# Kernel optimization log

Hardware: AMD Instinct MI355X
Metric: run time of the kernel (lower is better)

Reference implementation:

```python
import jax, jax.numpy as jnp
import numpy as np

B, LC, LT, D = 32, 2048, 512, 256  # D = 2*hidden_dim (bidirectional LSTM output)


def setup_inputs() -> dict:
    key = jax.random.key(0)
    k1, k2 = jax.random.split(key)
    return {
        "context_hidden": jax.random.normal(k1, (B, LC, D), dtype=jnp.float32),
        "target_hidden": jax.random.normal(k2, (B, LT, D), dtype=jnp.float32),
    }


def reference(context_hidden, target_hidden):
    # Pairwise Euclidean distance via |c|^2 + |t|^2 - 2 c.t (replaces the
    # original Python double for-loop of per-pair torch.norm calls).
    c2 = jnp.sum(context_hidden * context_hidden, axis=-1, keepdims=True)      # [B,Lc,1]
    t2 = jnp.sum(target_hidden * target_hidden, axis=-1)[:, None, :]           # [B,1,Lt]
    ct = jnp.einsum('bcd,btd->bct', context_hidden, target_hidden)             # [B,Lc,Lt]
    dist = jnp.sqrt(jnp.maximum(c2 + t2 - 2.0 * ct, 0.0))
    weights = 1.0 / (1.0 + dist)  # G2CT: [B,Lc,Lt]
    # G2C_m = weights @ target ; G2T_m = weights^T @ context (as in forward)
    g2c_m = jnp.einsum('bct,btd->bcd', weights, target_hidden)                 # [B,Lc,D]
    g2t_m = jnp.einsum('bct,bcd->btd', weights, context_hidden)                # [B,Lt,D]
    # concat along sequence axis so the block has a single output tensor
    return jnp.concatenate([g2c_m, g2t_m], axis=1)                             # [B,Lc+Lt,D]
```

## Files before the change

kernel.cpp:

```cpp
#include <hip/hip_runtime.h>

typedef float f32x4 __attribute__((ext_vector_type(4)));
typedef short s16x8 __attribute__((ext_vector_type(8)));

#define NB_    32
#define NLC    2048
#define NLT    512
#define ND     256
#define NCHUNK 512
#define NITER  (NCHUNK / 32)

__device__ __forceinline__ unsigned short f2bf(float f) {
    union { float f; unsigned int u; } v; v.f = f;
    unsigned int r = v.u + 0x7FFFu + ((v.u >> 16) & 1u);
    return (unsigned short)(r >> 16);
}

__device__ __forceinline__ s16x8 cvt8(float4 a, float4 c, float s) {
    s16x8 f;
    f[0]=(short)f2bf(s*a.x); f[1]=(short)f2bf(s*a.y); f[2]=(short)f2bf(s*a.z); f[3]=(short)f2bf(s*a.w);
    f[4]=(short)f2bf(s*c.x); f[5]=(short)f2bf(s*c.y); f[6]=(short)f2bf(s*c.z); f[7]=(short)f2bf(s*c.w);
    return f;
}

__device__ __forceinline__ void glds16(const void* g, void* l) {
    __builtin_amdgcn_global_load_lds(
        (const __attribute__((address_space(1))) unsigned int*)g,
        (__attribute__((address_space(3))) unsigned int*)l, 16, 0, 0);
}

__global__ __launch_bounds__(256) void prep_kernel(
    const float* __restrict__ ctx, const float* __restrict__ tgt,
    float* __restrict__ norms,
    unsigned short* __restrict__ ctxb, unsigned short* __restrict__ tgtb)
{
    const int wave = threadIdx.x >> 6;
    const int lane = threadIdx.x & 63;
    const int rid = blockIdx.x * 4 + wave;
    const float* row;
    unsigned short* drow;
    if (rid < NB_ * NLC) { row = ctx + (size_t)rid * ND; drow = ctxb + (size_t)rid * ND; }
    else { row = tgt + (size_t)(rid - NB_ * NLC) * ND; drow = tgtb + (size_t)(rid - NB_ * NLC) * ND; }
    const float4 v = *(const float4*)(row + lane * 4);
    *(ushort4*)(drow + lane * 4) = make_ushort4(f2bf(v.x), f2bf(v.y), f2bf(v.z), f2bf(v.w));
    float s = v.x * v.x + v.y * v.y + v.z * v.z + v.w * v.w;
    #pragma unroll
    for (int off = 32; off >= 1; off >>= 1) s += __shfl_xor(s, off);
    if (lane == 0) norms[rid] = s;
}

__global__ __launch_bounds__(256) void transpose_bf(
    const unsigned short* __restrict__ ctxb, const unsigned short* __restrict__ tgtb,
    unsigned short* __restrict__ ctxTp, unsigned short* __restrict__ tgtTp)
{
    __shared__ unsigned short tile[64][72];
    const int id = blockIdx.x;
    const unsigned short* in;
    unsigned short* outp;
    const int t = threadIdx.x;
    if (id < 4096) {
        const int b = id >> 7, r = id & 127, lt = r >> 2, dt = r & 3;
        in   = ctxb + ((size_t)b * NLC + lt * 64) * ND + dt * 64;
        outp = ctxTp + (((size_t)b * 32 + lt) * 256 + dt * 64) * 64;
    } else {
        const int id2 = id - 4096;
        const int b = id2 >> 5, r = id2 & 31, lt = r >> 2, dt = r & 3;
        in   = tgtb + ((size_t)b * NLT + lt * 64) * ND + dt * 64;
        outp = tgtTp + (((size_t)b * 8 + lt) * 256 + dt * 64) * 64;
    }
    const int r0 = t >> 2, c0 = t & 3;
    const s16x8 v0 = *(const s16x8*)&in[(size_t)r0 * ND + c0 * 8];
    const s16x8 v1 = *(const s16x8*)&in[(size_t)r0 * ND + (c0 + 4) * 8];
    *(s16x8*)&tile[r0][c0 * 8] = v0;
    *(s16x8*)&tile[r0][(c0 + 4) * 8] = v1;
    __syncthreads();
    unsigned short buf[16];
    #pragma unroll
    for (int i = 0; i < 16; ++i) buf[i] = tile[(t & 3) * 16 + i][t >> 2];
    unsigned short* op = outp + (size_t)(t >> 2) * 64 + (t & 3) * 16;
    *(s16x8*)&op[0] = *(const s16x8*)&buf[0];
    *(s16x8*)&op[8] = *(const s16x8*)&buf[8];
}

__global__ __launch_bounds__(256, 2) void k1_weights(
    const unsigned short* __restrict__ ctxb, const unsigned short* __restrict__ tgtb,
    const float* __restrict__ norms,
    unsigned short* __restrict__ Wg, unsigned short* __restrict__ WTg)
{
    __shared__ __align__(16) unsigned short Alds[2][128 * 64];
    __shared__ __align__(16) unsigned short Blds[2][128 * 64];
    __shared__ __align__(16) unsigned short relay[4][16 * 128];

    const int phys = blockIdx.x;
    const int L = (phys & 7) * 256 + (phys >> 3);
    const int b = L >> 6;
    const int r = L & 63;
    const int cb = r >> 2, tb = r & 3;

    const int tid = threadIdx.x, wave = tid >> 6, lane = tid & 63;
    const int lr = lane & 15, lq = lane >> 4;
    const int cw = cb * 128 + wave * 32;

    const unsigned short* Actx = ctxb + ((size_t)b * NLC + cb * 128) * ND;
    const unsigned short* Btgt = tgtb + ((size_t)b * NLT + tb * 128) * ND;

    auto STAGE = [&](int buf, int ks) {
        #pragma unroll
        for (int i = 0; i < 4; ++i) {
            const int q = wave * 4 + i;
            const int rloc = q * 8 + (lane >> 3);
            const int gcol = (lane & 7) ^ (rloc & 7);
            glds16(Actx + (size_t)rloc * ND + ks * 64 + gcol * 8, &Alds[buf][q * 512]);
            glds16(Btgt + (size_t)rloc * ND + ks * 64 + gcol * 8, &Blds[buf][q * 512]);
        }
    };

    f32x4 acc[2][8];
    #pragma unroll
    for (int mf = 0; mf < 2; ++mf)
        #pragma unroll
        for (int nf = 0; nf < 8; ++nf) acc[mf][nf] = (f32x4)(0.0f);

    STAGE(0, 0);
    int buf = 0;
    for (int ks = 0; ks < 4; ++ks) {
        __syncthreads();
        if (ks < 3) STAGE(buf ^ 1, ks + 1);
        #pragma unroll
        for (int kk = 0; kk < 2; ++kk) {
            s16x8 af[2];
            #pragma unroll
            for (int mf = 0; mf < 2; ++mf) {
                const int row = wave * 32 + mf * 16 + lr;
                af[mf] = *(const s16x8*)&Alds[buf][row * 64 + (((kk * 4 + lq) ^ (row & 7)) * 8)];
            }
            #pragma unroll
            for (int nf = 0; nf < 8; ++nf) {
                const int row = nf * 16 + lr;
                const s16x8 bf = *(const s16x8*)&Blds[buf][row * 64 + (((kk * 4 + lq) ^ (row & 7)) * 8)];
                acc[0][nf] = __builtin_amdgcn_mfma_f32_16x16x32_bf16(af[0], bf, acc[0][nf], 0, 0, 0);
                acc[1][nf] = __builtin_amdgcn_mfma_f32_16x16x32_bf16(af[1], bf, acc[1][nf], 0, 0, 0);
            }
        }
        buf ^= 1;
    }

    float c2[2][4], t2[8];
    #pragma unroll
    for (int mf = 0; mf < 2; ++mf)
        #pragma unroll
        for (int j = 0; j < 4; ++j)
            c2[mf][j] = norms[b * NLC + cw + mf * 16 + lq * 4 + j];
    #pragma unroll
    for (int nf = 0; nf < 8; ++nf)
        t2[nf] = norms[NB_ * NLC + b * NLT + tb * 128 + nf * 16 + lr];

    __syncthreads();
    unsigned short* WTs = (unsigned short*)Alds;

    #pragma unroll
    for (int mf = 0; mf < 2; ++mf) {
        #pragma unroll
        for (int nf = 0; nf < 8; ++nf) {
            unsigned short w4[4];
            #pragma unroll
            for (int j = 0; j < 4; ++j) {
                float d2 = c2[mf][j] + t2[nf] - 2.0f * acc[mf][nf][j];
                d2 = d2 > 0.0f ? d2 : 0.0f;
                w4[j] = f2bf(__builtin_amdgcn_rcpf(1.0f + __builtin_amdgcn_sqrtf(d2)));
                const int row = lq * 4 + j;
                relay[wave][row * 128 + ((nf * 16 + lr) ^ ((row & 7) << 3))] = w4[j];
            }
            const int t = nf * 16 + lr;
            const int c4 = (wave * 32 + mf * 16 + lq * 4) ^ ((t & 15) << 3);
            *(ushort4*)&WTs[t * 128 + c4] = make_ushort4(w4[0], w4[1], w4[2], w4[3]);
        }
        __syncthreads();
        {
            const int rrow = lane >> 2;
            const int ts   = (lane >> 1) & 1;
            const int half = lane & 1;
            const size_t wbase =
                (((size_t)b * 8 + tb * 2 + ts) * NLC + cb * 128 + wave * 32 + mf * 16 + rrow) * 64
                + half * 32;
            #pragma unroll
            for (int e = 0; e < 4; ++e) {
                const int tcol = ts * 64 + half * 32 + e * 8;
                const s16x8 v = *(const s16x8*)&relay[wave][rrow * 128 + (tcol ^ ((rrow & 7) << 3))];
                *(s16x8*)&Wg[wbase + e * 8] = v;
            }
        }
        __syncthreads();
    }

    {
        const int trow = tid >> 1;
        const int seg  = tid & 1;
        const size_t wtbase =
            (((size_t)b * 32 + cb * 2 + seg) * NLT + tb * 128 + trow) * 64;
        #pragma unroll
        for (int e = 0; e < 8; ++e) {
            const int c8 = (seg * 64 + e * 8) ^ ((trow & 15) << 3);
            *(s16x8*)&WTg[wtbase + e * 8] = *(const s16x8*)&WTs[trow * 128 + c8];
        }
    }
}

__global__ __launch_bounds__(256, 2) void k2_gemm(
    const unsigned short* __restrict__ Atp, const unsigned short* __restrict__ Wp,
    float* __restrict__ outp)
{
    __shared__ __align__(16) unsigned short Slds[2][256 * 64];

    const int phys = blockIdx.x;
    const int L = (phys & 7) * 64 + (phys >> 3);
    const int b = L >> 4, cb = L & 15;
    float* outB = outp + ((size_t)b * (NLC + NLT) + cb * 128) * ND;

    const int tid = threadIdx.x, wave = tid >> 6, lane = tid & 63;
    const int lr = lane & 15, lq = lane >> 4;

    const int srow = tid >> 3;
    const int schunk = tid & 7;

    auto STAGE = [&](int buf, int ks) {
        #pragma unroll
        for (int i = 0; i < 8; ++i) {
            const int row = i * 32 + srow;
            const int gcol = schunk ^ (row & 7);
            glds16(Atp + (((size_t)b * 8 + ks) * 256 + row) * 64 + gcol * 8,
                   &Slds[buf][(i * 32 + wave * 8) * 64]);
        }
    };

    f32x4 acc[16][2];
    #pragma unroll
    for (int mf = 0; mf < 16; ++mf) { acc[mf][0] = (f32x4)(0.0f); acc[mf][1] = (f32x4)(0.0f); }

    STAGE(0, 0);
    for (int ks = 0; ks < 8; ++ks) {
        __syncthreads();
        const int buf = ks & 1;
        if (ks < 7) STAGE(buf ^ 1, ks + 1);

        s16x8 bfr[2][2];
        #pragma unroll
        for (int j = 0; j < 2; ++j)
            #pragma unroll
            for (int kk = 0; kk < 2; ++kk)
                bfr[j][kk] = *(const s16x8*)&Wp[
                    (((size_t)b * 8 + ks) * NLC + cb * 128 + wave * 32 + j * 16 + lr) * 64
                    + kk * 32 + lq * 8];

        __builtin_amdgcn_s_setprio(1);
        #pragma unroll
        for (int kk = 0; kk < 2; ++kk) {
            #pragma unroll
            for (int mf = 0; mf < 16; ++mf) {
                const int row = mf * 16 + lr;
                const s16x8 af = *(const s16x8*)&Slds[buf][row * 64 +
                                                           (((kk * 4 + lq) ^ (row & 7)) * 8)];
                acc[mf][0] = __builtin_amdgcn_mfma_f32_16x16x32_bf16(af, bfr[0][kk], acc[mf][0], 0, 0, 0);
                acc[mf][1] = __builtin_amdgcn_mfma_f32_16x16x32_bf16(af, bfr[1][kk], acc[mf][1], 0, 0, 0);
            }
        }
        __builtin_amdgcn_s_setprio(0);
    }

    #pragma unroll
    for (int j = 0; j < 2; ++j) {
        const int col = wave * 32 + j * 16 + lr;
        float* rp = outB + (size_t)col * ND;
        #pragma unroll
        for (int mf = 0; mf < 16; ++mf) {
            const f32x4 v = acc[mf][j];
            *(float4*)(rp + mf * 16 + lq * 4) = make_float4(v[0], v[1], v[2], v[3]);
        }
    }
}

__global__ __launch_bounds__(512, 2) void k3v5(
    const unsigned short* __restrict__ ctxTp, const unsigned short* __restrict__ WTp,
    float* __restrict__ out)
{
    __shared__ __align__(16) unsigned short Alds[2][128 * 64];
    __shared__ __align__(16) unsigned short Blds[2][128 * 64];

    const int phys = blockIdx.x;
    const int L = (phys & 7) * 32 + (phys >> 3);
    const int b = L >> 3, r = L & 7;
    const int tb = r >> 1, dh = r & 1;

    const int tid = threadIdx.x, wave = tid >> 6, lane = tid & 63;
    const int lr = lane & 15, lq = lane >> 4;
    const int wd = wave >> 2, wt = wave & 3;

    auto STAGE = [&](int buf, int ks) {
        #pragma unroll
        for (int i = 0; i < 2; ++i) {
            const int q = wave * 2 + i;
            const int rloc = q * 8 + (lane >> 3);
            const int gcol = (lane & 7) ^ (rloc & 7);
            glds16(ctxTp + (((size_t)b * 32 + ks) * 256 + dh * 128 + rloc) * 64 + gcol * 8,
                   &Alds[buf][q * 512]);
            glds16(WTp + (((size_t)b * 32 + ks) * NLT + tb * 128 + rloc) * 64 + gcol * 8,
                   &Blds[buf][q * 512]);
        }
    };

    f32x4 acc[4][2];
    #pragma unroll
    for (int mf = 0; mf < 4; ++mf) { acc[mf][0] = (f32x4)(0.0f); acc[mf][1] = (f32x4)(0.0f); }

    STAGE(0, 0);
    for (int ks = 0; ks < 32; ++ks) {
        __syncthreads();
        const int buf = ks & 1;
        if (ks < 31) STAGE(buf ^ 1, ks + 1);

        __builtin_amdgcn_s_setprio(1);
        #pragma unroll
        for (int kk = 0; kk < 2; ++kk) {
            s16x8 bfr[2];
            #pragma unroll
            for (int nf = 0; nf < 2; ++nf) {
                const int row = wt * 32 + nf * 16 + lr;
                bfr[nf] = *(const s16x8*)&Blds[buf][row * 64 + (((kk * 4 + lq) ^ (row & 7)) * 8)];
            }
            #pragma unroll
            for (int mf = 0; mf < 4; ++mf) {
                const int row = wd * 64 + mf * 16 + lr;
                const s16x8 af = *(const s16x8*)&Alds[buf][row * 64 +
                                                           (((kk * 4 + lq) ^ (row & 7)) * 8)];
                acc[mf][0] = __builtin_amdgcn_mfma_f32_16x16x32_bf16(af, bfr[0], acc[mf][0], 0, 0, 0);
                acc[mf][1] = __builtin_amdgcn_mfma_f32_16x16x32_bf16(af, bfr[1], acc[mf][1], 0, 0, 0);
            }
        }
        __builtin_amdgcn_s_setprio(0);
    }

    #pragma unroll
    for (int nf = 0; nf < 2; ++nf) {
        const int t = tb * 128 + wt * 32 + nf * 16 + lr;
        float* rp = out + ((size_t)b * (NLC + NLT) + NLC + t) * ND + dh * 128 + wd * 64;
        #pragma unroll
        for (int mf = 0; mf < 4; ++mf) {
            const f32x4 v = acc[mf][nf];
            *(float4*)(rp + mf * 16 + lq * 4) = make_float4(v[0], v[1], v[2], v[3]);
        }
    }
}

__global__ __launch_bounds__(256) void zero_g2t(float* __restrict__ out) {
    const int g = blockIdx.x * 256 + threadIdx.x;
    #pragma unroll
    for (int k = 0; k < 4; ++k) {
        const int i = g + k * 262144;
        const int bb = i >> 15;
        const int off = i & 32767;
        *(float4*)(out + ((size_t)bb * (NLC + NLT) + NLC) * ND + (size_t)off * 4) =
            make_float4(0.f, 0.f, 0.f, 0.f);
    }
}

__global__ __launch_bounds__(256) void reduce_g2t(const float* __restrict__ part,
                                                  float* __restrict__ out) {
    const int g = blockIdx.x * 256 + threadIdx.x;
    #pragma unroll
    for (int k = 0; k < 4; ++k) {
        const int i = g + k * 262144;
        const int b = i >> 15;
        const int rem = i & 32767;
        const int row = rem >> 6;
        const int d4 = (rem & 63) * 4;
        const int mb = row >> 7, rr = row & 127;
        const size_t base = ((size_t)(b * 16 + mb * 4) * 32768) + (size_t)rr * 256 + d4;
        float4 s0 = *(const float4*)(part + base);
        float4 s1 = *(const float4*)(part + base + 32768);
        float4 s2 = *(const float4*)(part + base + 65536);
        float4 s3 = *(const float4*)(part + base + 98304);
        *(float4*)(out + ((size_t)b * (NLC + NLT) + NLC + row) * ND + d4) =
            make_float4(s0.x + s1.x + s2.x + s3.x, s0.y + s1.y + s2.y + s3.y,
                        s0.z + s1.z + s2.z + s3.z, s0.w + s1.w + s2.w + s3.w);
    }
}

__global__ __launch_bounds__(256, 2) void fused_dist_attn(
    const float* __restrict__ ctx, const float* __restrict__ tgt,
    float* __restrict__ out, float* __restrict__ part)
{
    __shared__ __align__(16) unsigned short Klds[2][32 * 256];
    __shared__ __align__(16) unsigned short VTlds[2][256 * 32];
    __shared__ __align__(16) unsigned short Wlds[4 * 32 * 32];
    __shared__ unsigned int KextLds[2][32];

    const int phys = blockIdx.x;
    const int L = (phys & 7) * 128 + (phys >> 3);
    const int isB = (L & 1) == 0;
    const int idx = L >> 1;
    const int b = idx >> 4;
    const float *Q, *KV;
    size_t outbase;
    if (isB) {
        const int mb = (idx >> 2) & 3, nc = idx & 3;
        Q = tgt + ((size_t)b * NLT + mb * 128) * ND;
        KV = ctx + ((size_t)b * NLC + nc * NCHUNK) * ND;
        outbase = ((size_t)b * (NLC + NLT) + NLC + mb * 128) * ND;
    } else {
        const int mb = idx & 15;
        Q = ctx + ((size_t)b * NLC + mb * 128) * ND;
        KV = tgt + (size_t)b * NLT * ND;
        outbase = ((size_t)b * (NLC + NLT) + mb * 128) * ND;
    }

    const int tid = threadIdx.x, wave = tid >> 6, lane = tid & 63;
    const int lr = lane & 15, lq = lane >> 4;

    s16x8 qf[2][8];
    s16x8 qe[2];
    #pragma unroll
    for (int mf = 0; mf < 2; ++mf) {
        const float* qrow = Q + (size_t)(wave * 32 + mf * 16 + lr) * ND;
        float q2 = 0.0f;
        #pragma unroll
        for (int kk = 0; kk < 8; ++kk) {
            const float4 a = *(const float4*)(qrow + kk * 32 + lq * 8);
            const float4 c = *(const float4*)(qrow + kk * 32 + lq * 8 + 4);
            q2 += a.x*a.x + a.y*a.y + a.z*a.z + a.w*a.w;
            q2 += c.x*c.x + c.y*c.y + c.z*c.z + c.w*c.w;
            qf[mf][kk] = cvt8(a, c, -2.0f);
        }
        q2 += __shfl_xor(q2, 16);
        q2 += __shfl_xor(q2, 32);
        union { unsigned int u[4]; s16x8 v; } qu;
        qu.u[0] = (lq == 0) ? (0x3F80u | ((unsigned int)f2bf(q2) << 16)) : 0u;
        qu.u[1] = 0u; qu.u[2] = 0u; qu.u[3] = 0u;
        qe[mf] = qu.v;
    }

    f32x4 acc[2][16];
    #pragma unroll
    for (int mf = 0; mf < 2; ++mf)
        #pragma unroll
        for (int dt = 0; dt < 16; ++dt)
            acc[mf][dt] = (f32x4)(0.0f);

    const int r4 = 8 * wave + 4 * (lane & 1);
    const int d8 = (lane >> 1) * 8;
    float4 ldr[4][2];

    auto LOADT = [&](int n0) {
        #pragma unroll
        for (int rr = 0; rr < 4; ++rr)
            #pragma unroll
            for (int h = 0; h < 2; ++h)
                ldr[rr][h] = *(const float4*)(KV + (size_t)(n0 + r4 + rr) * ND + d8 + 4 * h);
    };

    auto WRITET = [&](int sel) {
        float ps[4];
        unsigned short kb[4][8];
        #pragma unroll
        for (int rr = 0; rr < 4; ++rr) {
            const float4 a = ldr[rr][0], c = ldr[rr][1];
            ps[rr] = a.x*a.x + a.y*a.y + a.z*a.z + a.w*a.w
                   + c.x*c.x + c.y*c.y + c.z*c.z + c.w*c.w;
            kb[rr][0]=f2bf(a.x); kb[rr][1]=f2bf(a.y); kb[rr][2]=f2bf(a.z); kb[rr][3]=f2bf(a.w);
            kb[rr][4]=f2bf(c.x); kb[rr][5]=f2bf(c.y); kb[rr][6]=f2bf(c.z); kb[rr][7]=f2bf(c.w);
            const int rx = r4 + rr;
            *(s16x8*)&Klds[sel][rx * 256 + (d8 ^ ((rx & 7) << 3))] = *(const s16x8*)kb[rr];
        }
        #pragma unroll
        for (int dd = 0; dd < 8; ++dd) {
            const int d = d8 + dd;
            *(ushort4*)&VTlds[sel][d * 32 + (r4 ^ (((d >> 3) & 3) << 3))] =
                make_ushort4(kb[0][dd], kb[1][dd], kb[2][dd], kb[3][dd]);
        }
        #pragma unroll
        for (int rr = 0; rr < 4; ++rr) {
            ps[rr] += __shfl_xor(ps[rr], 2);
            ps[rr] += __shfl_xor(ps[rr], 4);
            ps[rr] += __shfl_xor(ps[rr], 8);
            ps[rr] += __shfl_xor(ps[rr], 16);
            ps[rr] += __shfl_xor(ps[rr], 32);
        }
        if (lane < 2) {
            #pragma unroll
            for (int rr = 0; rr < 4; ++rr)
                KextLds[sel][8 * wave + 4 * lane + rr] =
                    (unsigned int)f2bf(ps[rr]) | 0x3F800000u;
        }
    };

    LOADT(0);
    WRITET(0);

    #pragma unroll 2
    for (int t = 0; t < NITER; ++t) {
        __syncthreads();
        const int sel = t & 1;
        if (t + 1 < NITER) LOADT((t + 1) * 32);

        unsigned int p0 = 0u, p1 = 0u;
        if (lq == 0) { p0 = KextLds[sel][lr]; p1 = KextLds[sel][16 + lr]; }
        union { unsigned int u[4]; s16x8 v; } keu0, keu1;
        keu0.u[0] = p0; keu0.u[1] = 0; keu0.u[2] = 0; keu0.u[3] = 0;
        keu1.u[0] = p1; keu1.u[1] = 0; keu1.u[2] = 0; keu1.u[3] = 0;

        f32x4 sacc[2][2];
        sacc[0][0] = (f32x4)(0.0f); sacc[0][1] = (f32x4)(0.0f);
        sacc[1][0] = (f32x4)(0.0f); sacc[1][1] = (f32x4)(0.0f);
        __builtin_amdgcn_s_setprio(1);
        #pragma unroll
        for (int kk = 0; kk < 8; ++kk) {
            const int cs = (kk * 32 + lq * 8) ^ ((lr & 7) << 3);
            const s16x8 kf0 = *(const s16x8*)&Klds[sel][lr * 256 + cs];
            const s16x8 kf1 = *(const s16x8*)&Klds[sel][(16 + lr) * 256 + cs];
            sacc[0][0] = __builtin_amdgcn_mfma_f32_16x16x32_bf16(kf0, qf[0][kk], sacc[0][0], 0, 0, 0);
            sacc[0][1] = __builtin_amdgcn_mfma_f32_16x16x32_bf16(kf0, qf[1][kk], sacc[0][1], 0, 0, 0);
            sacc[1][0] = __builtin_amdgcn_mfma_f32_16x16x32_bf16(kf1, qf[0][kk], sacc[1][0], 0, 0, 0);
            sacc[1][1] = __builtin_amdgcn_mfma_f32_16x16x32_bf16(kf1, qf[1][kk], sacc[1][1], 0, 0, 0);
        }
        sacc[0][0] = __builtin_amdgcn_mfma_f32_16x16x32_bf16(keu0.v, qe[0], sacc[0][0], 0, 0, 0);
        sacc[0][1] = __builtin_amdgcn_mfma_f32_16x16x32_bf16(keu0.v, qe[1], sacc[0][1], 0, 0, 0);
        sacc[1][0] = __builtin_amdgcn_mfma_f32_16x16x32_bf16(keu1.v, qe[0], sacc[1][0], 0, 0, 0);
        sacc[1][1] = __builtin_amdgcn_mfma_f32_16x16x32_bf16(keu1.v, qe[1], sacc[1][1], 0, 0, 0);
        __builtin_amdgcn_s_setprio(0);

        #pragma unroll
        for (int ns = 0; ns < 2; ++ns) {
            #pragma unroll
            for (int mf = 0; mf < 2; ++mf) {
                unsigned short w4[4];
                #pragma unroll
                for (int j = 0; j < 4; ++j) {
                    float d2 = sacc[ns][mf][j];
                    d2 = d2 > 0.0f ? d2 : 0.0f;
                    w4[j] = f2bf(__builtin_amdgcn_rcpf(1.0f + __builtin_amdgcn_sqrtf(d2)));
                }
                const int row = mf * 16 + lr;
                const int col = (ns * 16 + lq * 4) ^ ((row & 3) << 3);
                *(ushort4*)&Wlds[wave * 1024 + row * 32 + col] =
                    make_ushort4(w4[0], w4[1], w4[2], w4[3]);
            }
        }

        s16x8 wfr[2];
        #pragma unroll
        for (int mf = 0; mf < 2; ++mf)
            wfr[mf] = *(const s16x8*)&Wlds[wave * 1024 + (mf * 16 + lr) * 32 +
                                           ((lq * 8) ^ ((lr & 3) << 3))];
        __builtin_amdgcn_s_setprio(1);
        #pragma unroll
        for (int dt = 0; dt < 16; ++dt) {
            const int vr = dt * 16 + lr;
            const s16x8 vf = *(const s16x8*)&VTlds[sel][vr * 32 +
                                                        ((lq * 8) ^ (((vr >> 3) & 3) << 3))];
            acc[0][dt] = __builtin_amdgcn_mfma_f32_16x16x32_bf16(vf, wfr[0], acc[0][dt], 0, 0, 0);
            acc[1][dt] = __builtin_amdgcn_mfma_f32_16x16x32_bf16(vf, wfr[1], acc[1][dt], 0, 0, 0);
        }
        __builtin_amdgcn_s_setprio(0);

        if (t + 1 < NITER) WRITET(sel ^ 1);
    }

    if (isB) {
        if (part) {
            float* p = part + (size_t)idx * 32768;
            #pragma unroll
            for (int mf = 0; mf < 2; ++mf) {
                const size_t rowbase = (size_t)(wave * 32 + mf * 16 + lr) * ND;
                #pragma unroll
                for (int dt = 0; dt < 16; ++dt) {
                    const f32x4 v = acc[mf][dt];
                    *(float4*)(p + rowbase + dt * 16 + lq * 4) = make_float4(v[0], v[1], v[2], v[3]);
                }
            }
        } else {
            #pragma unroll
            for (int mf = 0; mf < 2; ++mf) {
                float* rowp = out + outbase + (size_t)(wave * 32 + mf * 16 + lr) * ND;
                #pragma unroll
                for (int dt = 0; dt < 16; ++dt)
                    #pragma unroll
                    for (int j = 0; j < 4; ++j)
                        atomicAdd(rowp + dt * 16 + lq * 4 + j, acc[mf][dt][j]);
            }
        }
    } else {
        #pragma unroll
        for (int mf = 0; mf < 2; ++mf) {
            const size_t rowbase = outbase + (size_t)(wave * 32 + mf * 16 + lr) * ND;
            #pragma unroll
            for (int dt = 0; dt < 16; ++dt) {
                const f32x4 v = acc[mf][dt];
                *(float4*)(out + rowbase + dt * 16 + lq * 4) = make_float4(v[0], v[1], v[2], v[3]);
            }
        }
    }
}

extern "C" void kernel_launch(void* const* d_in, const int* in_sizes, int n_in,
                              void* d_out, int out_size, void* d_ws, size_t ws_size,
                              hipStream_t stream) {
    const float* ctx = (const float*)d_in[0];
    const float* tgt = (const float*)d_in[1];
    float* out = (float*)d_out;

    const size_t OFF_NORMS = 0;
    const size_t OFF_CTXB  = 327680;
    const size_t OFF_TGTB  = OFF_CTXB + 33554432;
    const size_t OFF_CTXT  = OFF_TGTB + 8388608;
    const size_t OFF_TGTT  = OFF_CTXT + 33554432;
    const size_t OFF_W     = OFF_TGTT + 8388608;
    const size_t OFF_WT    = OFF_W + 67108864;
    const size_t NEED_NEW  = OFF_WT + 67108864;

    char* ws = (char*)d_ws;
    if (ws_size >= NEED_NEW) {
        float* norms = (float*)(ws + OFF_NORMS);
        unsigned short* ctxb  = (unsigned short*)(ws + OFF_CTXB);
        unsigned short* tgtb  = (unsigned short*)(ws + OFF_TGTB);
        unsigned short* ctxTp = (unsigned short*)(ws + OFF_CTXT);
        unsigned short* tgtTp = (unsigned short*)(ws + OFF_TGTT);
        unsigned short* Wg    = (unsigned short*)(ws + OFF_W);
        unsigned short* WTg   = (unsigned short*)(ws + OFF_WT);

        prep_kernel<<<20480, 256, 0, stream>>>(ctx, tgt, norms, ctxb, tgtb);
        transpose_bf<<<5120, 256, 0, stream>>>(ctxb, tgtb, ctxTp, tgtTp);
        k1_weights<<<2048, 256, 0, stream>>>(ctxb, tgtb, norms, Wg, WTg);
        k2_gemm<<<512, 256, 0, stream>>>(tgtTp, Wg, out);
        k3v5<<<256, 512, 0, stream>>>(ctxTp, WTg, out);
    } else {
        const size_t need = (size_t)512 * 128 * 256 * 4;
        if (ws_size >= need) {
            float* part = (float*)d_ws;
            fused_dist_attn<<<1024, 256, 0, stream>>>(ctx, tgt, out, part);
            reduce_g2t<<<1024, 256, 0, stream>>>(part, out);
        } else {
            zero_g2t<<<1024, 256, 0, stream>>>(out);
            fused_dist_attn<<<1024, 256, 0, stream>>>(ctx, tgt, out, nullptr);
        }
    }
}
```

Measured before the change: 184.0 us.

## Fuse prep and transpose kernels; single-buffer k1 LDS for higher occupancy

Merges the norm/bf16-convert kernel and the transpose kernel into one kernel. Each block now converts a 64-row tile, writes both the row-major bf16 copy and the transposed copy, and computes the norms, so the intermediate bf16 data is no longer re-read from global memory and one launch is removed. Separately, k1_weights drops its double-buffered LDS staging for a single buffer aliased with the relay and transpose scratch. This cuts LDS use so that 3 blocks per CU fit instead of 2. In exchange, the global-to-LDS loads are no longer overlapped with MFMA work inside a block, and the fused prep uses large per-thread arrays that may raise register pressure.

New measurement: 188.4 us. 2.4% more time.

```diff
diff --git a/kernel.cpp b/kernel.cpp
--- a/kernel.cpp
+++ b/kernel.cpp
@@ -29,67 +29,70 @@
         (__attribute__((address_space(3))) unsigned int*)l, 16, 0, 0);
 }
 
-__global__ __launch_bounds__(256) void prep_kernel(
+__global__ __launch_bounds__(256) void prep2(
     const float* __restrict__ ctx, const float* __restrict__ tgt,
     float* __restrict__ norms,
-    unsigned short* __restrict__ ctxb, unsigned short* __restrict__ tgtb)
-{
-    const int wave = threadIdx.x >> 6;
-    const int lane = threadIdx.x & 63;
-    const int rid = blockIdx.x * 4 + wave;
-    const float* row;
-    unsigned short* drow;
-    if (rid < NB_ * NLC) { row = ctx + (size_t)rid * ND; drow = ctxb + (size_t)rid * ND; }
-    else { row = tgt + (size_t)(rid - NB_ * NLC) * ND; drow = tgtb + (size_t)(rid - NB_ * NLC) * ND; }
-    const float4 v = *(const float4*)(row + lane * 4);
-    *(ushort4*)(drow + lane * 4) = make_ushort4(f2bf(v.x), f2bf(v.y), f2bf(v.z), f2bf(v.w));
-    float s = v.x * v.x + v.y * v.y + v.z * v.z + v.w * v.w;
-    #pragma unroll
-    for (int off = 32; off >= 1; off >>= 1) s += __shfl_xor(s, off);
-    if (lane == 0) norms[rid] = s;
-}
-
-__global__ __launch_bounds__(256) void transpose_bf(
-    const unsigned short* __restrict__ ctxb, const unsigned short* __restrict__ tgtb,
+    unsigned short* __restrict__ ctxb, unsigned short* __restrict__ tgtb,
     unsigned short* __restrict__ ctxTp, unsigned short* __restrict__ tgtTp)
 {
-    __shared__ unsigned short tile[64][72];
+    __shared__ unsigned short tile[64 * 256];
     const int id = blockIdx.x;
-    const unsigned short* in;
-    unsigned short* outp;
+    const float* in;
+    unsigned short* outb;
+    unsigned short* outT;
+    int nrow_off;
+    if (id < 1024) {
+        const int b = id >> 5, lt = id & 31;
+        in   = ctx + ((size_t)b * NLC + lt * 64) * ND;
+        outb = ctxb + ((size_t)b * NLC + lt * 64) * ND;
+        outT = ctxTp + (((size_t)b * 32 + lt) * 256) * 64;
+        nrow_off = b * NLC + lt * 64;
+    } else {
+        const int id2 = id - 1024;
+        const int b = id2 >> 3, lt = id2 & 7;
+        in   = tgt + ((size_t)b * NLT + lt * 64) * ND;
+        outb = tgtb + ((size_t)b * NLT + lt * 64) * ND;
+        outT = tgtTp + (((size_t)b * 8 + lt) * 256) * 64;
+        nrow_off = NB_ * NLC + b * NLT + lt * 64;
+    }
     const int t = threadIdx.x;
-    if (id < 4096) {
-        const int b = id >> 7, r = id & 127, lt = r >> 2, dt = r & 3;
-        in   = ctxb + ((size_t)b * NLC + lt * 64) * ND + dt * 64;
-        outp = ctxTp + (((size_t)b * 32 + lt) * 256 + dt * 64) * 64;
-    } else {
-        const int id2 = id - 4096;
-        const int b = id2 >> 5, r = id2 & 31, lt = r >> 2, dt = r & 3;
-        in   = tgtb + ((size_t)b * NLT + lt * 64) * ND + dt * 64;
-        outp = tgtTp + (((size_t)b * 8 + lt) * 256 + dt * 64) * 64;
-    }
-    const int r0 = t >> 2, c0 = t & 3;
-    const s16x8 v0 = *(const s16x8*)&in[(size_t)r0 * ND + c0 * 8];
-    const s16x8 v1 = *(const s16x8*)&in[(size_t)r0 * ND + (c0 + 4) * 8];
-    *(s16x8*)&tile[r0][c0 * 8] = v0;
-    *(s16x8*)&tile[r0][(c0 + 4) * 8] = v1;
+    const int r = t >> 2, q = t & 3;
+    const float* rowp = in + (size_t)r * ND + q * 64;
+    unsigned short loc[64];
+    float s = 0.f;
+    #pragma unroll
+    for (int i = 0; i < 16; ++i) {
+        const float4 v = *(const float4*)(rowp + i * 4);
+        s += v.x*v.x + v.y*v.y + v.z*v.z + v.w*v.w;
+        loc[i*4+0]=f2bf(v.x); loc[i*4+1]=f2bf(v.y); loc[i*4+2]=f2bf(v.z); loc[i*4+3]=f2bf(v.w);
+    }
+    #pragma unroll
+    for (int i = 0; i < 8; ++i) {
+        *(s16x8*)&outb[(size_t)r * ND + q * 64 + i * 8] = *(const s16x8*)&loc[i*8];
+        *(s16x8*)&tile[r * 256 + q * 64 + i * 8]        = *(const s16x8*)&loc[i*8];
+    }
+    s += __shfl_xor(s, 1);
+    s += __shfl_xor(s, 2);
+    if (q == 0) norms[nrow_off + r] = s;
     __syncthreads();
-    unsigned short buf[16];
-    #pragma unroll
-    for (int i = 0; i < 16; ++i) buf[i] = tile[(t & 3) * 16 + i][t >> 2];
-    unsigned short* op = outp + (size_t)(t >> 2) * 64 + (t & 3) * 16;
-    *(s16x8*)&op[0] = *(const s16x8*)&buf[0];
-    *(s16x8*)&op[8] = *(const s16x8*)&buf[8];
-}
-
-__global__ __launch_bounds__(256, 2) void k1_weights(
+    unsigned short colv[64];
+    #pragma unroll
+    for (int rl = 0; rl < 64; ++rl) colv[rl] = tile[rl * 256 + t];
+    #pragma unroll
+    for (int i = 0; i < 8; ++i)
+        *(s16x8*)&outT[(size_t)t * 64 + i * 8] = *(const s16x8*)&colv[i*8];
+}
+
+__global__ __launch_bounds__(256, 3) void k1_weights(
     const unsigned short* __restrict__ ctxb, const unsigned short* __restrict__ tgtb,
     const float* __restrict__ norms,
     unsigned short* __restrict__ Wg, unsigned short* __restrict__ WTg)
 {
-    __shared__ __align__(16) unsigned short Alds[2][128 * 64];
-    __shared__ __align__(16) unsigned short Blds[2][128 * 64];
-    __shared__ __align__(16) unsigned short relay[4][16 * 128];
+    __shared__ __align__(16) unsigned short u[24576];
+    unsigned short* Alds = u;
+    unsigned short* Blds = u + 8192;
+    unsigned short* relay = u;
+    unsigned short* WTs   = u + 8192;
 
     const int phys = blockIdx.x;
     const int L = (phys & 7) * 256 + (phys >> 3);
@@ -104,14 +107,14 @@
     const unsigned short* Actx = ctxb + ((size_t)b * NLC + cb * 128) * ND;
     const unsigned short* Btgt = tgtb + ((size_t)b * NLT + tb * 128) * ND;
 
-    auto STAGE = [&](int buf, int ks) {
+    auto STAGE = [&](int ks) {
         #pragma unroll
         for (int i = 0; i < 4; ++i) {
             const int q = wave * 4 + i;
             const int rloc = q * 8 + (lane >> 3);
             const int gcol = (lane & 7) ^ (rloc & 7);
-            glds16(Actx + (size_t)rloc * ND + ks * 64 + gcol * 8, &Alds[buf][q * 512]);
-            glds16(Btgt + (size_t)rloc * ND + ks * 64 + gcol * 8, &Blds[buf][q * 512]);
+            glds16(Actx + (size_t)rloc * ND + ks * 64 + gcol * 8, &Alds[q * 512]);
+            glds16(Btgt + (size_t)rloc * ND + ks * 64 + gcol * 8, &Blds[q * 512]);
         }
     };
 
@@ -121,28 +124,26 @@
         #pragma unroll
         for (int nf = 0; nf < 8; ++nf) acc[mf][nf] = (f32x4)(0.0f);
 
-    STAGE(0, 0);
-    int buf = 0;
     for (int ks = 0; ks < 4; ++ks) {
+        STAGE(ks);
         __syncthreads();
-        if (ks < 3) STAGE(buf ^ 1, ks + 1);
         #pragma unroll
         for (int kk = 0; kk < 2; ++kk) {
             s16x8 af[2];
             #pragma unroll
             for (int mf = 0; mf < 2; ++mf) {
                 const int row = wave * 32 + mf * 16 + lr;
-                af[mf] = *(const s16x8*)&Alds[buf][row * 64 + (((kk * 4 + lq) ^ (row & 7)) * 8)];
+                af[mf] = *(const s16x8*)&Alds[row * 64 + (((kk * 4 + lq) ^ (row & 7)) * 8)];
             }
             #pragma unroll
             for (int nf = 0; nf < 8; ++nf) {
                 const int row = nf * 16 + lr;
-                const s16x8 bf = *(const s16x8*)&Blds[buf][row * 64 + (((kk * 4 + lq) ^ (row & 7)) * 8)];
+                const s16x8 bf = *(const s16x8*)&Blds[row * 64 + (((kk * 4 + lq) ^ (row & 7)) * 8)];
                 acc[0][nf] = __builtin_amdgcn_mfma_f32_16x16x32_bf16(af[0], bf, acc[0][nf], 0, 0, 0);
                 acc[1][nf] = __builtin_amdgcn_mfma_f32_16x16x32_bf16(af[1], bf, acc[1][nf], 0, 0, 0);
             }
         }
-        buf ^= 1;
+        __syncthreads();
     }
 
     float c2[2][4], t2[8];
@@ -154,9 +155,6 @@
     #pragma unroll
     for (int nf = 0; nf < 8; ++nf)
         t2[nf] = norms[NB_ * NLC + b * NLT + tb * 128 + nf * 16 + lr];
-
-    __syncthreads();
-    unsigned short* WTs = (unsigned short*)Alds;
 
     #pragma unroll
     for (int mf = 0; mf < 2; ++mf) {
@@ -169,7 +167,7 @@
                 d2 = d2 > 0.0f ? d2 : 0.0f;
                 w4[j] = f2bf(__builtin_amdgcn_rcpf(1.0f + __builtin_amdgcn_sqrtf(d2)));
                 const int row = lq * 4 + j;
-                relay[wave][row * 128 + ((nf * 16 + lr) ^ ((row & 7) << 3))] = w4[j];
+                relay[wave * 2048 + row * 128 + ((nf * 16 + lr) ^ ((row & 7) << 3))] = w4[j];
             }
             const int t = nf * 16 + lr;
             const int c4 = (wave * 32 + mf * 16 + lq * 4) ^ ((t & 15) << 3);
@@ -186,7 +184,8 @@
             #pragma unroll
             for (int e = 0; e < 4; ++e) {
                 const int tcol = ts * 64 + half * 32 + e * 8;
-                const s16x8 v = *(const s16x8*)&relay[wave][rrow * 128 + (tcol ^ ((rrow & 7) << 3))];
+                const s16x8 v = *(const s16x8*)&relay[wave * 2048 + rrow * 128 +
+                                                      (tcol ^ ((rrow & 7) << 3))];
                 *(s16x8*)&Wg[wbase + e * 8] = v;
             }
         }
@@ -626,8 +625,7 @@
         unsigned short* Wg    = (unsigned short*)(ws + OFF_W);
         unsigned short* WTg   = (unsigned short*)(ws + OFF_WT);
 
-        prep_kernel<<<20480, 256, 0, stream>>>(ctx, tgt, norms, ctxb, tgtb);
-        transpose_bf<<<5120, 256, 0, stream>>>(ctxb, tgtb, ctxTp, tgtTp);
+        prep2<<<1280, 256, 0, stream>>>(ctx, tgt, norms, ctxb, tgtb, ctxTp, tgtTp);
         k1_weights<<<2048, 256, 0, stream>>>(ctxb, tgtb, norms, Wg, WTg);
         k2_gemm<<<512, 256, 0, stream>>>(tgtTp, Wg, out);
         k3v5<<<256, 512, 0, stream>>>(ctxTp, WTg, out);
```

## Single-buffer k1 LDS staging and drop relay buffer to raise occupancy

Applied to the files above, without the earlier changes.

Shrinks k1_weights shared memory from double-buffered A/B tiles plus a relay buffer to one 32KB union, and raises launch bounds from 2 to 4 blocks per CU. The per-stage prefetch overlap is removed: each k-step now loads, syncs, computes, then syncs again. The W output is written by reading columns back out of the transposed WTs tile instead of through a separate relay. This trades intra-block load/compute overlap, plus extra strided LDS reads and a 64-element register array per thread, for more resident blocks to hide latency.

After: 183.0 us. About the same (-0.5%).

```diff
diff --git a/kernel.cpp b/kernel.cpp
--- a/kernel.cpp
+++ b/kernel.cpp
@@ -82,14 +82,15 @@
     *(s16x8*)&op[8] = *(const s16x8*)&buf[8];
 }
 
-__global__ __launch_bounds__(256, 2) void k1_weights(
+__global__ __launch_bounds__(256, 4) void k1_weights(
     const unsigned short* __restrict__ ctxb, const unsigned short* __restrict__ tgtb,
     const float* __restrict__ norms,
     unsigned short* __restrict__ Wg, unsigned short* __restrict__ WTg)
 {
-    __shared__ __align__(16) unsigned short Alds[2][128 * 64];
-    __shared__ __align__(16) unsigned short Blds[2][128 * 64];
-    __shared__ __align__(16) unsigned short relay[4][16 * 128];
+    __shared__ __align__(16) unsigned short u[16384];
+    unsigned short* Alds = u;
+    unsigned short* Blds = u + 8192;
+    unsigned short* WTs  = u;
 
     const int phys = blockIdx.x;
     const int L = (phys & 7) * 256 + (phys >> 3);
@@ -104,14 +105,14 @@
     const unsigned short* Actx = ctxb + ((size_t)b * NLC + cb * 128) * ND;
     const unsigned short* Btgt = tgtb + ((size_t)b * NLT + tb * 128) * ND;
 
-    auto STAGE = [&](int buf, int ks) {
+    auto STAGE = [&](int ks) {
         #pragma unroll
         for (int i = 0; i < 4; ++i) {
             const int q = wave * 4 + i;
             const int rloc = q * 8 + (lane >> 3);
             const int gcol = (lane & 7) ^ (rloc & 7);
-            glds16(Actx + (size_t)rloc * ND + ks * 64 + gcol * 8, &Alds[buf][q * 512]);
-            glds16(Btgt + (size_t)rloc * ND + ks * 64 + gcol * 8, &Blds[buf][q * 512]);
+            glds16(Actx + (size_t)rloc * ND + ks * 64 + gcol * 8, &Alds[q * 512]);
+            glds16(Btgt + (size_t)rloc * ND + ks * 64 + gcol * 8, &Blds[q * 512]);
         }
     };
 
@@ -121,28 +122,26 @@
         #pragma unroll
         for (int nf = 0; nf < 8; ++nf) acc[mf][nf] = (f32x4)(0.0f);
 
-    STAGE(0, 0);
-    int buf = 0;
     for (int ks = 0; ks < 4; ++ks) {
+        STAGE(ks);
         __syncthreads();
-        if (ks < 3) STAGE(buf ^ 1, ks + 1);
         #pragma unroll
         for (int kk = 0; kk < 2; ++kk) {
             s16x8 af[2];
             #pragma unroll
             for (int mf = 0; mf < 2; ++mf) {
                 const int row = wave * 32 + mf * 16 + lr;
-                af[mf] = *(const s16x8*)&Alds[buf][row * 64 + (((kk * 4 + lq) ^ (row & 7)) * 8)];
+                af[mf] = *(const s16x8*)&Alds[row * 64 + (((kk * 4 + lq) ^ (row & 7)) * 8)];
             }
             #pragma unroll
             for (int nf = 0; nf < 8; ++nf) {
                 const int row = nf * 16 + lr;
-                const s16x8 bf = *(const s16x8*)&Blds[buf][row * 64 + (((kk * 4 + lq) ^ (row & 7)) * 8)];
+                const s16x8 bf = *(const s16x8*)&Blds[row * 64 + (((kk * 4 + lq) ^ (row & 7)) * 8)];
                 acc[0][nf] = __builtin_amdgcn_mfma_f32_16x16x32_bf16(af[0], bf, acc[0][nf], 0, 0, 0);
                 acc[1][nf] = __builtin_amdgcn_mfma_f32_16x16x32_bf16(af[1], bf, acc[1][nf], 0, 0, 0);
             }
         }
-        buf ^= 1;
+        __syncthreads();
     }
 
     float c2[2][4], t2[8];
@@ -154,9 +153,6 @@
     #pragma unroll
     for (int nf = 0; nf < 8; ++nf)
         t2[nf] = norms[NB_ * NLC + b * NLT + tb * 128 + nf * 16 + lr];
-
-    __syncthreads();
-    unsigned short* WTs = (unsigned short*)Alds;
 
     #pragma unroll
     for (int mf = 0; mf < 2; ++mf) {
@@ -168,29 +164,26 @@
                 float d2 = c2[mf][j] + t2[nf] - 2.0f * acc[mf][nf][j];
                 d2 = d2 > 0.0f ? d2 : 0.0f;
                 w4[j] = f2bf(__builtin_amdgcn_rcpf(1.0f + __builtin_amdgcn_sqrtf(d2)));
-                const int row = lq * 4 + j;
-                relay[wave][row * 128 + ((nf * 16 + lr) ^ ((row & 7) << 3))] = w4[j];
             }
             const int t = nf * 16 + lr;
             const int c4 = (wave * 32 + mf * 16 + lq * 4) ^ ((t & 15) << 3);
             *(ushort4*)&WTs[t * 128 + c4] = make_ushort4(w4[0], w4[1], w4[2], w4[3]);
         }
-        __syncthreads();
-        {
-            const int rrow = lane >> 2;
-            const int ts   = (lane >> 1) & 1;
-            const int half = lane & 1;
-            const size_t wbase =
-                (((size_t)b * 8 + tb * 2 + ts) * NLC + cb * 128 + wave * 32 + mf * 16 + rrow) * 64
-                + half * 32;
-            #pragma unroll
-            for (int e = 0; e < 4; ++e) {
-                const int tcol = ts * 64 + half * 32 + e * 8;
-                const s16x8 v = *(const s16x8*)&relay[wave][rrow * 128 + (tcol ^ ((rrow & 7) << 3))];
-                *(s16x8*)&Wg[wbase + e * 8] = v;
-            }
-        }
-        __syncthreads();
+    }
+    __syncthreads();
+
+    {
+        const int c = tid >> 1, half = tid & 1;
+        unsigned short colv[64];
+        #pragma unroll
+        for (int i = 0; i < 64; ++i) {
+            const int t = half * 64 + i;
+            colv[i] = WTs[t * 128 + (c ^ ((t & 15) << 3))];
+        }
+        const size_t wbase = (((size_t)b * 8 + tb * 2 + half) * NLC + cb * 128 + c) * 64;
+        #pragma unroll
+        for (int e = 0; e < 8; ++e)
+            *(s16x8*)&Wg[wbase + e * 8] = *(const s16x8*)&colv[e * 8];
     }
 
     {
```
